# Optimization experiments

Hardware: AMD Instinct MI355X
Metric: run time of the kernel (lower is better)

The kernel has to match this reference:

```python
import jax, jax.numpy as jnp
import numpy as np
from jax import lax

H = 64  # hidden_size

def _lstm_layer(x, w_ih, w_hh, b_ih, b_hh):
    # x: (B, T, in). PyTorch gate order [i, f, g, o]; gates = x@W_ih^T + h@W_hh^T + b_ih + b_hh.
    B, T, _ = x.shape
    xw = jnp.einsum('bti,gi->btg', x, w_ih) + (b_ih + b_hh)  # (B, T, 4H), input projection hoisted out of scan

    def step(carry, xw_t):
        h, c = carry
        gates = xw_t + h @ w_hh.T                     # (B, 4H)
        i, f, g, o = jnp.split(gates, 4, axis=-1)
        i = jax.nn.sigmoid(i)
        f = jax.nn.sigmoid(f)
        g = jnp.tanh(g)
        o = jax.nn.sigmoid(o)
        c = f * c + i * g
        h = o * jnp.tanh(c)
        return (h, c), h

    h0 = jnp.zeros((B, H), dtype=x.dtype)
    c0 = jnp.zeros((B, H), dtype=x.dtype)
    (h_n, _), hs = lax.scan(step, (h0, c0), jnp.swapaxes(xw, 0, 1))  # hs: (T, B, H)
    return jnp.swapaxes(hs, 0, 1), h_n


def setup_inputs() -> dict:
    key = jax.random.key(0)
    ks = jax.random.split(key, 12)
    s = 1.0 / np.sqrt(H)  # PyTorch LSTM init scale
    return {
        'x':     jax.random.normal(ks[0], (2048, 512, 4), dtype=jnp.float32),
        'w_ih0': jax.random.uniform(ks[1], (4 * H, 4), jnp.float32, -s, s),
        'w_hh0': jax.random.uniform(ks[2], (4 * H, H), jnp.float32, -s, s),
        'b_ih0': jax.random.uniform(ks[3], (4 * H,), jnp.float32, -s, s),
        'b_hh0': jax.random.uniform(ks[4], (4 * H,), jnp.float32, -s, s),
        'w_ih1': jax.random.uniform(ks[5], (4 * H, H), jnp.float32, -s, s),
        'w_hh1': jax.random.uniform(ks[6], (4 * H, H), jnp.float32, -s, s),
        'b_ih1': jax.random.uniform(ks[7], (4 * H,), jnp.float32, -s, s),
        'b_hh1': jax.random.uniform(ks[8], (4 * H,), jnp.float32, -s, s),
        'fc_w':  jax.random.uniform(ks[9], (H, H), jnp.float32, -s, s),
        'fc_b':  jax.random.uniform(ks[10], (H,), jnp.float32, -s, s),
    }


def reference(x, w_ih0, w_hh0, b_ih0, b_hh0, w_ih1, w_hh1, b_ih1, b_hh1, fc_w, fc_b):
    # 2-layer LSTM (eval mode: inter-layer dropout inactive), take last layer's final hidden,
    # then Linear + tanh.
    h1_seq, _ = _lstm_layer(x, w_ih0, w_hh0, b_ih0, b_hh0)
    _, h_n = _lstm_layer(h1_seq, w_ih1, w_hh1, b_ih1, b_hh1)
    return jnp.tanh(h_n @ fc_w.T + fc_b)
```

## Files before the change

### kernel.cpp

```cpp
#include <hip/hip_runtime.h>


#define HID 64
#define TSTEPS 512
#define MB 8
#define BLK 512
#define HSTR 88
#define LOG2E  1.4426950408889634f
#define LOG2E2 2.8853900817779268f

typedef _Float16 f16;
typedef _Float16 half8 __attribute__((ext_vector_type(8)));
typedef _Float16 half4 __attribute__((ext_vector_type(4)));
typedef float f32x4 __attribute__((ext_vector_type(4)));

__device__ __forceinline__ float tanh2(float y) {
    return fmaf(2.0f, __builtin_amdgcn_rcpf(1.0f + __builtin_amdgcn_exp2f(-y)), -1.0f);
}

__global__ __launch_bounds__(BLK, 2) void lstm_mfma(
    const float* __restrict__ x,
    const float* __restrict__ w_ih0,
    const float* __restrict__ w_hh0,
    const float* __restrict__ b_ih0,
    const float* __restrict__ b_hh0,
    const float* __restrict__ w_ih1,
    const float* __restrict__ w_hh1,
    const float* __restrict__ b_ih1,
    const float* __restrict__ b_hh1,
    const float* __restrict__ fc_w,
    const float* __restrict__ fc_b,
    float* __restrict__ out)
{
    __shared__ f16 xs[TSTEPS * MB * 4];
    __shared__ f16 h0s[2][MB * HSTR];
    __shared__ f16 h1s[2][MB * HSTR];

    const int tid  = threadIdx.x;
    const int w    = tid >> 6;
    const int l    = tid & 63;
    const int quad = l >> 4;
    const int l15  = l & 15;
    const int wl   = w & 3;
    const bool isL0 = (w < 4);
    const int b0   = blockIdx.x * MB;

    const int RM = (l15 < 8) ? l15 : ((l15 & 4) | ((l15 + 2) & 3));

    for (int it = tid; it < MB * TSTEPS; it += BLK) {
        const int m = it >> 9;
        const int t = it & 511;
        const float4 v = *((const float4*)x + (size_t)(b0 + m) * TSTEPS + t);
        *(half4*)(xs + (t * MB + m) * 4) =
            (half4){ (f16)v.x, (f16)v.y, (f16)v.z, (f16)v.w };
    }
    for (int it = tid; it < MB * HSTR; it += BLK) {
        h0s[0][it] = (f16)0.f; h0s[1][it] = (f16)0.f;
        h1s[0][it] = (f16)0.f; h1s[1][it] = (f16)0.f;
    }

    half8 Bf[4][4];
    f32x4 biasv[4];
    const half8 Z = { (f16)0.f,(f16)0.f,(f16)0.f,(f16)0.f,
                      (f16)0.f,(f16)0.f,(f16)0.f,(f16)0.f };
    #pragma unroll
    for (int ti = 0; ti < 4; ++ti) {
        const int n = (wl + 4 * ti) * 16 + l15;
        const float sc = (ti == 2) ? LOG2E2 : LOG2E;
        float bval;
        if (isL0) {
            bval = (b_ih0[n] + b_hh0[n]) * sc;
            half8 pz = Z;
            if (quad == 0) {
                const float4 v = *(const float4*)(w_ih0 + n * 4);
                pz[0] = (f16)(v.x * sc); pz[1] = (f16)(v.y * sc);
                pz[2] = (f16)(v.z * sc); pz[3] = (f16)(v.w * sc);
            }
            Bf[ti][0] = pz;
            #pragma unroll
            for (int ks = 0; ks < 2; ++ks) {
                const int ko = ks * 32 + quad * 8;
                const float4 a = *(const float4*)(w_hh0 + n * HID + ko);
                const float4 b = *(const float4*)(w_hh0 + n * HID + ko + 4);
                Bf[ti][1 + ks] = (half8){
                    (f16)(a.x*sc),(f16)(a.y*sc),(f16)(a.z*sc),(f16)(a.w*sc),
                    (f16)(b.x*sc),(f16)(b.y*sc),(f16)(b.z*sc),(f16)(b.w*sc) };
            }
            Bf[ti][3] = Z;
        } else {
            bval = (b_ih1[n] + b_hh1[n]) * sc;
            #pragma unroll
            for (int ks = 0; ks < 2; ++ks) {
                const int ko = ks * 32 + quad * 8;
                const float4 a = *(const float4*)(w_ih1 + n * HID + ko);
                const float4 b = *(const float4*)(w_ih1 + n * HID + ko + 4);
                Bf[ti][ks] = (half8){
                    (f16)(a.x*sc),(f16)(a.y*sc),(f16)(a.z*sc),(f16)(a.w*sc),
                    (f16)(b.x*sc),(f16)(b.y*sc),(f16)(b.z*sc),(f16)(b.w*sc) };
                const float4 c = *(const float4*)(w_hh1 + n * HID + ko);
                const float4 d = *(const float4*)(w_hh1 + n * HID + ko + 4);
                Bf[ti][2 + ks] = (half8){
                    (f16)(c.x*sc),(f16)(c.y*sc),(f16)(c.z*sc),(f16)(c.w*sc),
                    (f16)(d.x*sc),(f16)(d.y*sc),(f16)(d.z*sc),(f16)(d.w*sc) };
            }
        }
        biasv[ti] = (f32x4){ bval, bval, bval, bval };
    }

    const int  mrow = (quad & 1) * 4 + (quad & 2);
    const int  uu   = wl * 16 + l15;
    const int  hb   = RM * HSTR + quad * 8;
    float cst0 = 0.f, cst1 = 0.f;
    f32x4 g[4];

    auto load_x = [&](int r) -> half4 {
        return *(const half4*)(xs + (r * MB + RM) * 4);
    };
    auto l0_mfma = [&](half4 xv, const f16* h0rd) {
        __builtin_amdgcn_s_setprio(1);
        half8 ax = Z;
        if (quad == 0) { ax[0]=xv[0]; ax[1]=xv[1]; ax[2]=xv[2]; ax[3]=xv[3]; }
        const half8 A1 = *(const half8*)(h0rd + hb);
        const half8 A2 = *(const half8*)(h0rd + hb + 32);
        #pragma unroll
        for (int ti = 0; ti < 4; ++ti) {
            f32x4 acc;
            acc   = __builtin_amdgcn_mfma_f32_16x16x32_f16(ax, Bf[ti][0], biasv[ti], 0, 0, 0);
            acc   = __builtin_amdgcn_mfma_f32_16x16x32_f16(A1, Bf[ti][1], acc, 0, 0, 0);
            g[ti] = __builtin_amdgcn_mfma_f32_16x16x32_f16(A2, Bf[ti][2], acc, 0, 0, 0);
        }
        __builtin_amdgcn_s_setprio(0);
    };
    auto l1_mfma = [&](const f16* h0rd, const f16* h1rd) {
        const half8 A1 = *(const half8*)(h0rd + hb);
        const half8 A2 = *(const half8*)(h0rd + hb + 32);
        const half8 A3 = *(const half8*)(h1rd + hb);
        const half8 A4 = *(const half8*)(h1rd + hb + 32);
        #pragma unroll
        for (int ti = 0; ti < 4; ++ti) {
            f32x4 acc;
            acc   = __builtin_amdgcn_mfma_f32_16x16x32_f16(A1, Bf[ti][0], biasv[ti], 0, 0, 0);
            acc   = __builtin_amdgcn_mfma_f32_16x16x32_f16(A2, Bf[ti][1], acc, 0, 0, 0);
            acc   = __builtin_amdgcn_mfma_f32_16x16x32_f16(A3, Bf[ti][2], acc, 0, 0, 0);
            g[ti] = __builtin_amdgcn_mfma_f32_16x16x32_f16(A4, Bf[ti][3], acc, 0, 0, 0);
        }
    };
    auto act_store = [&](f16* dst) {
        #pragma unroll
        for (int j = 0; j < 2; ++j) {
            const float ei = __builtin_amdgcn_exp2f(-g[0][j]);
            const float ef = __builtin_amdgcn_exp2f(-g[1][j]);
            const float eg = __builtin_amdgcn_exp2f(-g[2][j]);
            const float eo = __builtin_amdgcn_exp2f(-g[3][j]);
            float& c = j ? cst1 : cst0;
            const float af = 1.0f + ef;
            const float P  = (1.0f + ei) * (1.0f + eg);
            const float N  = fmaf(c * P, 1.0f, (1.0f - eg) * af);
            c = N * __builtin_amdgcn_rcpf(P * af);
            const float ym = fminf(-LOG2E2 * c, 126.0f);
            const float ec = __builtin_amdgcn_exp2f(ym);
            const float r2 = __builtin_amdgcn_rcpf((1.0f + eo) * (1.0f + ec));
            dst[(mrow + j) * HSTR + uu] = (f16)((1.0f - ec) * r2);
        }
    };

    __syncthreads();

    half4 xv;
    if (isL0) xv = load_x(0);
    if (isL0) { l0_mfma(xv, h0s[1]); act_store(h0s[0]); xv = load_x(1); }
    __syncthreads();
    if (isL0) { l0_mfma(xv, h0s[0]); act_store(h0s[1]); xv = load_x(2); }
    else      { l1_mfma(h0s[0], h1s[1]); act_store(h1s[0]); }
    __syncthreads();

    #pragma unroll 1
    for (int r = 2; r < 510; r += 2) {
        if (isL0) { l0_mfma(xv, h0s[1]); act_store(h0s[0]); xv = load_x(r + 1); }
        else      { l1_mfma(h0s[1], h1s[0]); act_store(h1s[1]); }
        __syncthreads();
        if (isL0) { l0_mfma(xv, h0s[0]); act_store(h0s[1]); xv = load_x(r + 2); }
        else      { l1_mfma(h0s[0], h1s[1]); act_store(h1s[0]); }
        __syncthreads();
    }
    if (isL0) { l0_mfma(xv, h0s[1]); act_store(h0s[0]); xv = load_x(511); }
    else      { l1_mfma(h0s[1], h1s[0]); act_store(h1s[1]); }
    __syncthreads();
    if (isL0) { l0_mfma(xv, h0s[0]); act_store(h0s[1]); }
    else      { l1_mfma(h0s[0], h1s[1]); act_store(h1s[0]); }
    __syncthreads();
    if (!isL0) { l1_mfma(h0s[1], h1s[0]); act_store(h1s[1]); }
    __syncthreads();

    {
        const int v = tid & 63;
        const int m = tid >> 6;
        float a = fc_b[v];
        const f16* hp = h1s[1] + m * HSTR;
        const float4* wp = (const float4*)(fc_w + v * HID);
        #pragma unroll
        for (int kk = 0; kk < HID / 4; ++kk) {
            const float4 wv = wp[kk];
            a += (float)hp[kk * 4 + 0] * wv.x + (float)hp[kk * 4 + 1] * wv.y
               + (float)hp[kk * 4 + 2] * wv.z + (float)hp[kk * 4 + 3] * wv.w;
        }
        out[(size_t)(b0 + m) * HID + v] = tanh2(a * LOG2E2);
    }
}

extern "C" void kernel_launch(void* const* d_in, const int* in_sizes, int n_in,
                              void* d_out, int out_size, void* d_ws, size_t ws_size,
                              hipStream_t stream) {
    const float* x     = (const float*)d_in[0];
    const float* w_ih0 = (const float*)d_in[1];
    const float* w_hh0 = (const float*)d_in[2];
    const float* b_ih0 = (const float*)d_in[3];
    const float* b_hh0 = (const float*)d_in[4];
    const float* w_ih1 = (const float*)d_in[5];
    const float* w_hh1 = (const float*)d_in[6];
    const float* b_ih1 = (const float*)d_in[7];
    const float* b_hh1 = (const float*)d_in[8];
    const float* fc_w  = (const float*)d_in[9];
    const float* fc_b  = (const float*)d_in[10];
    float* out = (float*)d_out;

    const int B = in_sizes[0] / (TSTEPS * 4);
    lstm_mfma<<<dim3(B / MB), dim3(BLK), 0, stream>>>(
        x, w_ih0, w_hh0, b_ih0, b_hh0, w_ih1, w_hh1, b_ih1, b_hh1, fc_w, fc_b, out);
}
```

Measured before the change: 327.2 us.

## Compute layer-0 input projection with FMAs from global x and batch reciprocals

Removes the shared-memory staging of x and the extra MFMA that applied the input projection in layer 0. Each lane instead loads its two batch rows of x straight from global memory each step and folds x·W_ih plus bias into the accumulator with scalar FMAs. It also pairs the two rows' reciprocals into one rcp each for the cell and output paths, and lowers the exp clamp. This trims per-step MFMA latency and LDS, at the cost of global loads inside the serial loop and slightly different float rounding.

```diff
diff --git a/kernel.cpp b/kernel.cpp
--- a/kernel.cpp
+++ b/kernel.cpp
@@ -32,7 +32,6 @@
     const float* __restrict__ fc_b,
     float* __restrict__ out)
 {
-    __shared__ f16 xs[TSTEPS * MB * 4];
     __shared__ f16 h0s[2][MB * HSTR];
     __shared__ f16 h1s[2][MB * HSTR];
 
@@ -47,13 +46,6 @@
 
     const int RM = (l15 < 8) ? l15 : ((l15 & 4) | ((l15 + 2) & 3));
 
-    for (int it = tid; it < MB * TSTEPS; it += BLK) {
-        const int m = it >> 9;
-        const int t = it & 511;
-        const float4 v = *((const float4*)x + (size_t)(b0 + m) * TSTEPS + t);
-        *(half4*)(xs + (t * MB + m) * 4) =
-            (half4){ (f16)v.x, (f16)v.y, (f16)v.z, (f16)v.w };
-    }
     for (int it = tid; it < MB * HSTR; it += BLK) {
         h0s[0][it] = (f16)0.f; h0s[1][it] = (f16)0.f;
         h1s[0][it] = (f16)0.f; h1s[1][it] = (f16)0.f;
@@ -61,34 +53,27 @@
 
     half8 Bf[4][4];
     f32x4 biasv[4];
-    const half8 Z = { (f16)0.f,(f16)0.f,(f16)0.f,(f16)0.f,
-                      (f16)0.f,(f16)0.f,(f16)0.f,(f16)0.f };
+    float b0s[4];
+    float4 w0f[4];
     #pragma unroll
     for (int ti = 0; ti < 4; ++ti) {
         const int n = (wl + 4 * ti) * 16 + l15;
         const float sc = (ti == 2) ? LOG2E2 : LOG2E;
-        float bval;
         if (isL0) {
-            bval = (b_ih0[n] + b_hh0[n]) * sc;
-            half8 pz = Z;
-            if (quad == 0) {
-                const float4 v = *(const float4*)(w_ih0 + n * 4);
-                pz[0] = (f16)(v.x * sc); pz[1] = (f16)(v.y * sc);
-                pz[2] = (f16)(v.z * sc); pz[3] = (f16)(v.w * sc);
-            }
-            Bf[ti][0] = pz;
+            b0s[ti] = (b_ih0[n] + b_hh0[n]) * sc;
+            const float4 wv = *(const float4*)(w_ih0 + n * 4);
+            w0f[ti] = (float4){ wv.x * sc, wv.y * sc, wv.z * sc, wv.w * sc };
             #pragma unroll
             for (int ks = 0; ks < 2; ++ks) {
                 const int ko = ks * 32 + quad * 8;
                 const float4 a = *(const float4*)(w_hh0 + n * HID + ko);
                 const float4 b = *(const float4*)(w_hh0 + n * HID + ko + 4);
-                Bf[ti][1 + ks] = (half8){
+                Bf[ti][ks] = (half8){
                     (f16)(a.x*sc),(f16)(a.y*sc),(f16)(a.z*sc),(f16)(a.w*sc),
                     (f16)(b.x*sc),(f16)(b.y*sc),(f16)(b.z*sc),(f16)(b.w*sc) };
             }
-            Bf[ti][3] = Z;
         } else {
-            bval = (b_ih1[n] + b_hh1[n]) * sc;
+            const float bval = (b_ih1[n] + b_hh1[n]) * sc;
             #pragma unroll
             for (int ks = 0; ks < 2; ++ks) {
                 const int ko = ks * 32 + quad * 8;
@@ -103,8 +88,8 @@
                     (f16)(c.x*sc),(f16)(c.y*sc),(f16)(c.z*sc),(f16)(c.w*sc),
                     (f16)(d.x*sc),(f16)(d.y*sc),(f16)(d.z*sc),(f16)(d.w*sc) };
             }
-        }
-        biasv[ti] = (f32x4){ bval, bval, bval, bval };
+            biasv[ti] = (f32x4){ bval, bval, bval, bval };
+        }
     }
 
     const int  mrow = (quad & 1) * 4 + (quad & 2);
@@ -113,21 +98,28 @@
     float cst0 = 0.f, cst1 = 0.f;
     f32x4 g[4];
 
-    auto load_x = [&](int r) -> half4 {
-        return *(const half4*)(xs + (r * MB + RM) * 4);
-    };
-    auto l0_mfma = [&](half4 xv, const f16* h0rd) {
+    const float4* xp = (const float4*)x;
+    const size_t xrow_a = (size_t)(b0 + mrow) * TSTEPS;
+    const size_t xrow_b = xrow_a + TSTEPS;
+    float4 xa, xb;
+
+    auto l0_mfma = [&](const f16* h0rd) {
         __builtin_amdgcn_s_setprio(1);
-        half8 ax = Z;
-        if (quad == 0) { ax[0]=xv[0]; ax[1]=xv[1]; ax[2]=xv[2]; ax[3]=xv[3]; }
         const half8 A1 = *(const half8*)(h0rd + hb);
         const half8 A2 = *(const half8*)(h0rd + hb + 32);
         #pragma unroll
         for (int ti = 0; ti < 4; ++ti) {
-            f32x4 acc;
-            acc   = __builtin_amdgcn_mfma_f32_16x16x32_f16(ax, Bf[ti][0], biasv[ti], 0, 0, 0);
-            acc   = __builtin_amdgcn_mfma_f32_16x16x32_f16(A1, Bf[ti][1], acc, 0, 0, 0);
-            g[ti] = __builtin_amdgcn_mfma_f32_16x16x32_f16(A2, Bf[ti][2], acc, 0, 0, 0);
+            float c0 = fmaf(xa.x, w0f[ti].x, b0s[ti]);
+            c0 = fmaf(xa.y, w0f[ti].y, c0);
+            c0 = fmaf(xa.z, w0f[ti].z, c0);
+            c0 = fmaf(xa.w, w0f[ti].w, c0);
+            float c1 = fmaf(xb.x, w0f[ti].x, b0s[ti]);
+            c1 = fmaf(xb.y, w0f[ti].y, c1);
+            c1 = fmaf(xb.z, w0f[ti].z, c1);
+            c1 = fmaf(xb.w, w0f[ti].w, c1);
+            f32x4 acc = (f32x4){ c0, c1, c0, c1 };
+            acc   = __builtin_amdgcn_mfma_f32_16x16x32_f16(A1, Bf[ti][0], acc, 0, 0, 0);
+            g[ti] = __builtin_amdgcn_mfma_f32_16x16x32_f16(A2, Bf[ti][1], acc, 0, 0, 0);
         }
         __builtin_amdgcn_s_setprio(0);
     };
@@ -145,48 +137,57 @@
             g[ti] = __builtin_amdgcn_mfma_f32_16x16x32_f16(A4, Bf[ti][3], acc, 0, 0, 0);
         }
     };
+    auto load_x = [&](int r) {
+        xa = xp[xrow_a + r];
+        xb = xp[xrow_b + r];
+    };
     auto act_store = [&](f16* dst) {
-        #pragma unroll
-        for (int j = 0; j < 2; ++j) {
-            const float ei = __builtin_amdgcn_exp2f(-g[0][j]);
-            const float ef = __builtin_amdgcn_exp2f(-g[1][j]);
-            const float eg = __builtin_amdgcn_exp2f(-g[2][j]);
-            const float eo = __builtin_amdgcn_exp2f(-g[3][j]);
-            float& c = j ? cst1 : cst0;
-            const float af = 1.0f + ef;
-            const float P  = (1.0f + ei) * (1.0f + eg);
-            const float N  = fmaf(c * P, 1.0f, (1.0f - eg) * af);
-            c = N * __builtin_amdgcn_rcpf(P * af);
-            const float ym = fminf(-LOG2E2 * c, 126.0f);
-            const float ec = __builtin_amdgcn_exp2f(ym);
-            const float r2 = __builtin_amdgcn_rcpf((1.0f + eo) * (1.0f + ec));
-            dst[(mrow + j) * HSTR + uu] = (f16)((1.0f - ec) * r2);
-        }
-    };
-
-    __syncthreads();
-
-    half4 xv;
-    if (isL0) xv = load_x(0);
-    if (isL0) { l0_mfma(xv, h0s[1]); act_store(h0s[0]); xv = load_x(1); }
-    __syncthreads();
-    if (isL0) { l0_mfma(xv, h0s[0]); act_store(h0s[1]); xv = load_x(2); }
+        float e0[4], e1[4];
+        #pragma unroll
+        for (int t = 0; t < 4; ++t) {
+            e0[t] = __builtin_amdgcn_exp2f(-g[t][0]);
+            e1[t] = __builtin_amdgcn_exp2f(-g[t][1]);
+        }
+        const float af0 = 1.0f + e0[1],            af1 = 1.0f + e1[1];
+        const float P0  = (1.0f + e0[0]) * (1.0f + e0[2]);
+        const float P1  = (1.0f + e1[0]) * (1.0f + e1[2]);
+        const float N0  = fmaf(cst0, P0, (1.0f - e0[2]) * af0);
+        const float N1  = fmaf(cst1, P1, (1.0f - e1[2]) * af1);
+        const float D0  = P0 * af0,                D1  = P1 * af1;
+        const float rD  = __builtin_amdgcn_rcpf(D0 * D1);
+        cst0 = N0 * (rD * D1);
+        cst1 = N1 * (rD * D0);
+        const float ec0 = __builtin_amdgcn_exp2f(fminf(-LOG2E2 * cst0, 60.0f));
+        const float ec1 = __builtin_amdgcn_exp2f(fminf(-LOG2E2 * cst1, 60.0f));
+        const float E0  = (1.0f + e0[3]) * (1.0f + ec0);
+        const float E1  = (1.0f + e1[3]) * (1.0f + ec1);
+        const float rE  = __builtin_amdgcn_rcpf(E0 * E1);
+        dst[(mrow + 0) * HSTR + uu] = (f16)((1.0f - ec0) * (rE * E1));
+        dst[(mrow + 1) * HSTR + uu] = (f16)((1.0f - ec1) * (rE * E0));
+    };
+
+    if (isL0) load_x(0);
+    __syncthreads();
+
+    if (isL0) { l0_mfma(h0s[1]); load_x(1); act_store(h0s[0]); }
+    __syncthreads();
+    if (isL0) { l0_mfma(h0s[0]); load_x(2); act_store(h0s[1]); }
     else      { l1_mfma(h0s[0], h1s[1]); act_store(h1s[0]); }
     __syncthreads();
 
     #pragma unroll 1
     for (int r = 2; r < 510; r += 2) {
-        if (isL0) { l0_mfma(xv, h0s[1]); act_store(h0s[0]); xv = load_x(r + 1); }
+        if (isL0) { l0_mfma(h0s[1]); load_x(r + 1); act_store(h0s[0]); }
         else      { l1_mfma(h0s[1], h1s[0]); act_store(h1s[1]); }
         __syncthreads();
-        if (isL0) { l0_mfma(xv, h0s[0]); act_store(h0s[1]); xv = load_x(r + 2); }
+        if (isL0) { l0_mfma(h0s[0]); load_x(r + 2); act_store(h0s[1]); }
         else      { l1_mfma(h0s[0], h1s[1]); act_store(h1s[0]); }
         __syncthreads();
     }
-    if (isL0) { l0_mfma(xv, h0s[1]); act_store(h0s[0]); xv = load_x(511); }
+    if (isL0) { l0_mfma(h0s[1]); load_x(511); act_store(h0s[0]); }
     else      { l1_mfma(h0s[1], h1s[0]); act_store(h1s[1]); }
     __syncthreads();
-    if (isL0) { l0_mfma(xv, h0s[0]); act_store(h0s[1]); }
+    if (isL0) { l0_mfma(h0s[0]); act_store(h0s[1]); }
     else      { l1_mfma(h0s[0], h1s[1]); act_store(h1s[0]); }
     __syncthreads();
     if (!isL0) { l1_mfma(h0s[1], h1s[0]); act_store(h1s[1]); }
```

Result: slower. 379.3 us (+15.9%).
